# Optimization experiments

Measured on AMD Instinct MI355X. Metric: run time of the kernel, lower is better.

## Reference

```python
import jax, jax.numpy as jnp
import numpy as np

N_NODES = 40000
N_EDGES = 640000
IN_CH = 64
HID = 128
N_LAYERS = 3


def _linear_params(key, shape_in, shape_out):
    kw, kb = jax.random.split(key)
    lim = 1.0 / np.sqrt(shape_in)
    W = jax.random.uniform(kw, (shape_in, shape_out), jnp.float32, -lim, lim)
    b = jax.random.uniform(kb, (shape_out,), jnp.float32, -lim, lim)
    return W, b


def setup_inputs() -> dict:
    key = jax.random.key(0)
    ks = jax.random.split(key, 32)
    edge_index = jax.random.randint(ks[0], (2, N_EDGES), 0, N_NODES, dtype=jnp.int64 if jax.config.jax_enable_x64 else jnp.int32)
    x = jax.random.normal(ks[1], (N_NODES, IN_CH), jnp.float32)
    pos = jax.random.normal(ks[2], (N_NODES, 3), jnp.float32)
    emb_W, emb_b = _linear_params(ks[3], IN_CH, HID)

    def stack(fn):
        outs = [fn(l) for l in range(N_LAYERS)]
        Ws = jnp.stack([o[0] for o in outs])
        bs = jnp.stack([o[1] for o in outs])
        return Ws, bs

    # edge MLP: Linear(2H+1, H), SiLU, Linear(H, H), SiLU
    edge_W1, edge_b1 = stack(lambda l: _linear_params(ks[4 + l], 2 * HID + 1, HID))
    edge_W2, edge_b2 = stack(lambda l: _linear_params(ks[8 + l], HID, HID))
    # node MLP: Linear(2H, H), SiLU, Linear(H, H)
    node_W1, node_b1 = stack(lambda l: _linear_params(ks[12 + l], 2 * HID, HID))
    node_W2, node_b2 = stack(lambda l: _linear_params(ks[16 + l], HID, HID))
    # pos MLP: Linear(H, H), SiLU, Linear(H, 1)
    pos_W1, pos_b1 = stack(lambda l: _linear_params(ks[20 + l], HID, HID))
    pos_W2, pos_b2 = stack(lambda l: _linear_params(ks[24 + l], HID, 1))
    return {
        "edge_index": edge_index, "x": x, "pos": pos,
        "emb_W": emb_W, "emb_b": emb_b,
        "edge_W1": edge_W1, "edge_b1": edge_b1, "edge_W2": edge_W2, "edge_b2": edge_b2,
        "node_W1": node_W1, "node_b1": node_b1, "node_W2": node_W2, "node_b2": node_b2,
        "pos_W1": pos_W1, "pos_b1": pos_b1, "pos_W2": pos_W2, "pos_b2": pos_b2,
    }


def reference(edge_index, x, pos, emb_W, emb_b,
              edge_W1, edge_b1, edge_W2, edge_b2,
              node_W1, node_b1, node_W2, node_b2,
              pos_W1, pos_b1, pos_W2, pos_b2):
    silu = jax.nn.silu
    N = x.shape[0]
    src, dst = edge_index[0], edge_index[1]  # messages flow src -> dst
    # node embedding
    h = x @ emb_W + emb_b  # [N, H]
    # in-degree for mean aggregation of position updates
    deg = jnp.clip(jax.ops.segment_sum(jnp.ones(src.shape[0], pos.dtype), dst, num_segments=N), 1.0)
    L = edge_W1.shape[0]
    for l in range(L):
        h_i = h[dst]            # [E, H] target features
        h_j = h[src]            # [E, H] source features
        rel = pos[dst] - pos[src]  # [E, 3]
        d2 = jnp.sum(rel * rel, axis=-1, keepdims=True)  # [E, 1] squared distance
        e_in = jnp.concatenate([h_i, h_j, d2], axis=-1)  # [E, 2H+1]
        m = silu(silu(e_in @ edge_W1[l] + edge_b1[l]) @ edge_W2[l] + edge_b2[l])  # [E, H]
        agg = jax.ops.segment_sum(m, dst, num_segments=N)  # [N, H]
        n_in = jnp.concatenate([h, agg], axis=-1)  # [N, 2H]
        h = silu(n_in @ node_W1[l] + node_b1[l]) @ node_W2[l] + node_b2[l]
        # equivariant position update: pos_i += mean_j (pos_i - pos_j) * phi_x(m_ij)
        w = silu(m @ pos_W1[l] + pos_b1[l]) @ pos_W2[l] + pos_b2[l]  # [E, 1]
        pos = pos + jax.ops.segment_sum(rel * w, dst, num_segments=N) / deg[:, None]
    return h, pos
```

## Files before the change

### kernel.cpp

```cpp
#include <hip/hip_runtime.h>
#include <hip/hip_bf16.h>

#define N_NODES 40000
#define N_EDGES 640000
#define IN_CH 64
#define HID 128
#define N_LAYERS 3

typedef unsigned short u16;
typedef unsigned int u32;

typedef __attribute__((ext_vector_type(8))) __bf16 bf16x8;
typedef __attribute__((ext_vector_type(4))) float float4v;

__device__ __forceinline__ float bf2f(u16 u) {
    union { u32 i; float f; } v; v.i = ((u32)u) << 16; return v.f;
}
__device__ __forceinline__ float bflo(u32 p) {
    union { u32 i; float f; } v; v.i = p << 16; return v.f;
}
__device__ __forceinline__ float bfhi(u32 p) {
    union { u32 i; float f; } v; v.i = p & 0xffff0000u; return v.f;
}
__device__ __forceinline__ u16 f2bf(float f) {
    union { float f; u32 i; } v; v.f = f;
    u32 i = v.i;
    u32 r = (i + 0x7fffu + ((i >> 16) & 1u)) >> 16;
    return (u16)r;
}
__device__ __forceinline__ float silu_f(float x) {
    float d = 1.0f + __expf(-x);
#if __has_builtin(__builtin_amdgcn_rcpf)
    return x * __builtin_amdgcn_rcpf(d);
#else
    return __fdividef(x, d);
#endif
}

#define W_STRIDE 72
__device__ __forceinline__ void stage_w64(const u16* __restrict__ g, u16* s, int t,
                                          int chunk, int rowstride_u32) {
    const u32* gp = (const u32*)g;
    u32* sp = (u32*)s;
#pragma unroll
    for (int it = 0; it < 4; ++it) {
        int i4 = t + it * 256;
        int n = i4 >> 3, j = i4 & 7;
        *(uint4*)(sp + n * 36 + j * 4) = *(const uint4*)(gp + n * rowstride_u32 + chunk * 32 + j * 4);
    }
}
__device__ __forceinline__ void stage_w32_256(const u16* __restrict__ g, u16* s, int t, int chunk) {
    const u32* gp = (const u32*)g;
    u32* sp = (u32*)s;
#pragma unroll
    for (int it = 0; it < 4; ++it) {
        int i4 = t + it * 256;
        int o = i4 >> 2, j = i4 & 3;
        *(uint4*)(sp + o * 20 + j * 4) = *(const uint4*)(gp + o * 64 + chunk * 16 + j * 4);
    }
}

__global__ void detect_kernel(const void* __restrict__ w_raw,
                              const void* __restrict__ eidx_raw,
                              int* __restrict__ flags) {
    __shared__ int s_big, s_hi;
    if (threadIdx.x == 0) { s_big = 0; s_hi = 0; }
    __syncthreads();
    const u16* w16 = (const u16*)w_raw;
    for (int i = threadIdx.x; i < 8192; i += blockDim.x) {
        float v = bf2f(w16[i]);
        if (!(fabsf(v) <= 1.0f)) s_big = 1;
    }
    const u32* e32 = (const u32*)eidx_raw;
    for (int i = threadIdx.x; i < 256; i += blockDim.x) {
        if (e32[2 * i + 1] != 0u) s_hi = 1;
    }
    __syncthreads();
    if (threadIdx.x == 0) {
        flags[0] = s_big ? 0 : 1;
        flags[1] = s_hi ? 0 : 1;
    }
}

__global__ void cvt_f_kernel(const void* __restrict__ in, float* __restrict__ out,
                             int n, const int* __restrict__ flags) {
    int i = blockIdx.x * blockDim.x + threadIdx.x;
    if (i >= n) return;
    out[i] = flags[0] ? bf2f(((const u16*)in)[i]) : ((const float*)in)[i];
}

__global__ void cvt_idx_kernel(const void* __restrict__ in, int* __restrict__ out,
                               int n, const int* __restrict__ flags) {
    int i = blockIdx.x * blockDim.x + threadIdx.x;
    if (i >= n) return;
    out[i] = flags[1] ? (int)(((const long long*)in)[i]) : ((const int*)in)[i];
}

__global__ void tcvt_kernel(const void* __restrict__ in, u16* __restrict__ out,
                            int count, int kshift, int inLS, int outLS,
                            const int* __restrict__ flags) {
    int l = blockIdx.y;
    int i = blockIdx.x * blockDim.x + threadIdx.x;
    if (i >= count) return;
    int n = i >> kshift, k = i & ((1 << kshift) - 1);
    int si = inLS * l + k * HID + n;
    float v = flags[0] ? bf2f(((const u16*)in)[si]) : ((const float*)in)[si];
    out[(size_t)outLS * l + i] = f2bf(v);
}

__global__ void w1ab_kernel(const void* __restrict__ in, u16* __restrict__ out,
                            const int* __restrict__ flags) {
    int l = blockIdx.y;
    int i = blockIdx.x * blockDim.x + threadIdx.x;
    int o = i >> 7, k = i & 127;
    int si = l * (257 * 128) + ((o < 128) ? (k * 128 + o) : ((128 + k) * 128 + (o - 128)));
    float v = flags[0] ? bf2f(((const u16*)in)[si]) : ((const float*)in)[si];
    out[(size_t)l * 32768 + i] = f2bf(v);
}

__global__ void w1row_kernel(const void* __restrict__ in, float* __restrict__ out,
                             const int* __restrict__ flags) {
    int i = blockIdx.x * blockDim.x + threadIdx.x;
    if (i >= 384) return;
    int l = i >> 7, n = i & 127;
    int si = l * (257 * 128) + 256 * 128 + n;
    out[i] = flags[0] ? bf2f(((const u16*)in)[si]) : ((const float*)in)[si];
}

__global__ void cnt_kernel(const int* __restrict__ dst, int* __restrict__ cnt) {
    int e = blockIdx.x * blockDim.x + threadIdx.x;
    if (e < N_EDGES) atomicAdd(&cnt[dst[e]], 1);
}

__global__ __launch_bounds__(1024) void scan_kernel(const int* __restrict__ cnt,
                                                    int* __restrict__ offs) {
    __shared__ int s_part[1024];
    const int t = threadIdx.x;
    const int base = t * 40;
    int sum = 0;
    for (int j = 0; j < 40; ++j) {
        int idx = base + j;
        sum += (idx < N_NODES) ? cnt[idx] : 0;
    }
    s_part[t] = sum;
    __syncthreads();
    for (int d = 1; d < 1024; d <<= 1) {
        int v = (t >= d) ? s_part[t - d] : 0;
        __syncthreads();
        s_part[t] += v;
        __syncthreads();
    }
    int run = (t == 0) ? 0 : s_part[t - 1];
    for (int j = 0; j < 40; ++j) {
        int idx = base + j;
        if (idx < N_NODES) { offs[idx] = run; run += cnt[idx]; }
    }
    if (t == 1023) offs[N_NODES] = run;
}

__global__ void scatter_kernel(const int* __restrict__ src, const int* __restrict__ dst,
                               const int* __restrict__ offs, int* __restrict__ cur,
                               int* __restrict__ ssrc, int* __restrict__ sdst) {
    int e = blockIdx.x * blockDim.x + threadIdx.x;
    if (e >= N_EDGES) return;
    int n = dst[e];
    int p = offs[n] + atomicAdd(&cur[n], 1);
    ssrc[p] = src[e];
    sdst[p] = n;
}

__global__ void posinit_kernel(const void* __restrict__ pos_raw, float* __restrict__ posf,
                               const int* __restrict__ flags) {
    int i = blockIdx.x * blockDim.x + threadIdx.x;
    if (i < N_NODES * 3)
        posf[i] = flags[0] ? bf2f(((const u16*)pos_raw)[i]) : ((const float*)pos_raw)[i];
}

__global__ __launch_bounds__(64) void embed_kernel(
    const void* __restrict__ x_raw, const float* __restrict__ W, const float* __restrict__ b,
    u16* __restrict__ h, const int* __restrict__ flags)
{
    __shared__ float s_x[IN_CH];
    const int n = blockIdx.x;
    const int t = threadIdx.x;
    const int isbf = flags[0];
    s_x[t] = isbf ? bf2f(((const u16*)x_raw)[n * IN_CH + t])
                  : ((const float*)x_raw)[n * IN_CH + t];
    __syncthreads();
    const int o = 2 * t;
    float a0 = b[o], a1 = b[o + 1];
#pragma unroll 8
    for (int i = 0; i < IN_CH; ++i) {
        float xi = s_x[i];
        float2 w = *(const float2*)(W + i * HID + o);
        a0 = fmaf(xi, w.x, a0);
        a1 = fmaf(xi, w.y, a1);
    }
    *(u32*)(h + (size_t)n * HID + o) = (u32)f2bf(a0) | ((u32)f2bf(a1) << 16);
}

#define ACT_STRIDE 136

__global__ __launch_bounds__(256, 4) void uv_kernel(
    const u16* __restrict__ h, const u16* __restrict__ W1abt, const float* __restrict__ b1,
    u16* __restrict__ uv)
{
    __shared__ __align__(16) u16 s_a[64 * ACT_STRIDE];
    __shared__ __align__(16) u16 s_w[256 * 40];

    const int t = threadIdx.x;
    const int n0 = blockIdx.x * 64;
    const int wv = t >> 6, lane = t & 63, quad = lane >> 4, li = lane & 15;
    const int rowA = wv * 16 + li;
    const int rowC = wv * 16 + quad * 4;

    {
        int nl = t >> 2, part = t & 3;
        const uint4* hp = (const uint4*)((const u32*)h + (size_t)(n0 + nl) * 64 + part * 16);
        uint4* ap = (uint4*)((u32*)s_a + nl * (ACT_STRIDE / 2) + part * 16);
#pragma unroll
        for (int j = 0; j < 4; ++j) ap[j] = hp[j];
    }

    float4v acc[16];
#pragma unroll
    for (int ct = 0; ct < 16; ++ct) {
        float bias = (ct < 8) ? b1[ct * 16 + li] : 0.0f;
#pragma unroll
        for (int r = 0; r < 4; ++r) acc[ct][r] = bias;
    }

#pragma unroll
    for (int c = 0; c < 4; ++c) {
        if (c) __syncthreads();
        stage_w32_256(W1abt, s_w, t, c);
        __syncthreads();
        const bf16x8 av = *(const bf16x8*)(s_a + rowA * ACT_STRIDE + c * 32 + quad * 8);
#pragma unroll
        for (int ct = 0; ct < 16; ++ct) {
            const bf16x8 bv = *(const bf16x8*)(s_w + (ct * 16 + li) * 40 + quad * 8);
            acc[ct] = __builtin_amdgcn_mfma_f32_16x16x32_bf16(av, bv, acc[ct], 0, 0, 0);
        }
    }

#pragma unroll
    for (int ct = 0; ct < 16; ++ct) {
        int col = ct * 16 + li;
#pragma unroll
        for (int r = 0; r < 4; ++r)
            uv[(size_t)(n0 + rowC + r) * 256 + col] = f2bf(acc[ct][r]);
    }
}

#define TILE_E 64

__global__ __launch_bounds__(256, 4) void edge_mfma_kernel(
    const int* __restrict__ ssrc, const int* __restrict__ sdst,
    const u16* __restrict__ uv, const float* __restrict__ posf,
    const float* __restrict__ w1c_g,
    const u16* __restrict__ W2t, const float* __restrict__ b2,
    const u16* __restrict__ pW1t, const float* __restrict__ pb1,
    const float* __restrict__ pW2, const float* __restrict__ pb2,
    float* __restrict__ agg, float* __restrict__ pd)
{
    __shared__ __align__(16) u16 s_act[TILE_E * ACT_STRIDE];
    __shared__ __align__(16) u16 s_w[128 * W_STRIDE];
    __shared__ float s_w1c[128];
    __shared__ float s_d2[TILE_E];
    __shared__ float s_rel[TILE_E * 3];
    __shared__ int s_dstn[TILE_E], s_srcn[TILE_E];

    const int t = threadIdx.x;
    const int e0 = blockIdx.x * TILE_E;
    const int wv = t >> 6, lane = t & 63, quad = lane >> 4, li = lane & 15;
    const int rowA = wv * 16 + li;
    const int rowC = wv * 16 + quad * 4;

    if (t < TILE_E) {
        int e = e0 + t;
        int sN = ssrc[e], dN = sdst[e];
        s_dstn[t] = dN; s_srcn[t] = sN;
        float r0 = posf[dN * 3 + 0] - posf[sN * 3 + 0];
        float r1 = posf[dN * 3 + 1] - posf[sN * 3 + 1];
        float r2 = posf[dN * 3 + 2] - posf[sN * 3 + 2];
        s_rel[t * 3 + 0] = r0; s_rel[t * 3 + 1] = r1; s_rel[t * 3 + 2] = r2;
        s_d2[t] = r0 * r0 + r1 * r1 + r2 * r2;
    }
    if (t < 128) s_w1c[t] = w1c_g[t];
    stage_w64(W2t, s_w, t, 0, 64);
    __syncthreads();

    {
        int el = t >> 2, part = t & 3;
        int dN = s_dstn[el], sN = s_srcn[el];
        const uint4* up = (const uint4*)((const u32*)uv + (size_t)dN * 128 + part * 16);
        const uint4* vp = (const uint4*)((const u32*)uv + (size_t)sN * 128 + 64 + part * 16);
        float d2 = s_d2[el];
        u32* outp = (u32*)s_act + el * (ACT_STRIDE / 2) + part * 16;
        const float* wc = s_w1c + part * 32;
#pragma unroll
        for (int q4 = 0; q4 < 4; ++q4) {
            uint4 uu = up[q4];
            uint4 vv = vp[q4];
            u32 res[4];
#pragma unroll
            for (int j = 0; j < 4; ++j) {
                u32 ua = ((const u32*)&uu)[j], va = ((const u32*)&vv)[j];
                int col = q4 * 8 + j * 2;
                float x0 = fmaf(d2, wc[col],     bflo(ua) + bflo(va));
                float x1 = fmaf(d2, wc[col + 1], bfhi(ua) + bfhi(va));
                res[j] = (u32)f2bf(silu_f(x0)) | ((u32)f2bf(silu_f(x1)) << 16);
            }
            *(uint4*)(outp + q4 * 4) = *(uint4*)res;
        }
    }
    __syncthreads();

    float4v acc[8];
#pragma unroll
    for (int c = 0; c < 8; ++c) {
        float bias = b2[c * 16 + li];
#pragma unroll
        for (int r = 0; r < 4; ++r) acc[c][r] = bias;
    }
#pragma unroll
    for (int p = 0; p < 2; ++p) {
        if (p) {
            __syncthreads();
            stage_w64(W2t, s_w, t, 1, 64);
            __syncthreads();
        }
#pragma unroll
        for (int kk2 = 0; kk2 < 2; ++kk2) {
            const bf16x8 av = *(const bf16x8*)(s_act + rowA * ACT_STRIDE + p * 64 + kk2 * 32 + quad * 8);
#pragma unroll
            for (int c = 0; c < 8; ++c) {
                const bf16x8 bv = *(const bf16x8*)(s_w + (c * 16 + li) * W_STRIDE + kk2 * 32 + quad * 8);
                acc[c] = __builtin_amdgcn_mfma_f32_16x16x32_bf16(av, bv, acc[c], 0, 0, 0);
            }
        }
    }
    __syncthreads();

#pragma unroll
    for (int c = 0; c < 8; ++c) {
        int col = c * 16 + li;
#pragma unroll
        for (int r = 0; r < 4; ++r)
            s_act[(rowC + r) * ACT_STRIDE + col] = f2bf(silu_f(acc[c][r]));
    }
    stage_w64(pW1t, s_w, t, 0, 64);
    __syncthreads();

    {
        int c32 = t & 63, grp = t >> 6;
        int r0 = grp * 16;
        float run0 = 0.f, run1 = 0.f;
        int cur = s_dstn[r0];
        for (int r = r0; r < r0 + 16; ++r) {
            int dn = s_dstn[r];
            if (dn != cur) {
                atomicAdd(&agg[(size_t)cur * HID + 2 * c32], run0);
                atomicAdd(&agg[(size_t)cur * HID + 2 * c32 + 1], run1);
                run0 = run1 = 0.f; cur = dn;
            }
            u32 mm = *((const u32*)s_act + r * (ACT_STRIDE / 2) + c32);
            run0 += bflo(mm);
            run1 += bfhi(mm);
        }
        atomicAdd(&agg[(size_t)cur * HID + 2 * c32], run0);
        atomicAdd(&agg[(size_t)cur * HID + 2 * c32 + 1], run1);
    }

#pragma unroll
    for (int c = 0; c < 8; ++c) {
        float bias = pb1[c * 16 + li];
#pragma unroll
        for (int r = 0; r < 4; ++r) acc[c][r] = bias;
    }
#pragma unroll
    for (int p = 0; p < 2; ++p) {
        if (p) {
            __syncthreads();
            stage_w64(pW1t, s_w, t, 1, 64);
            __syncthreads();
        }
#pragma unroll
        for (int kk2 = 0; kk2 < 2; ++kk2) {
            const bf16x8 av = *(const bf16x8*)(s_act + rowA * ACT_STRIDE + p * 64 + kk2 * 32 + quad * 8);
#pragma unroll
            for (int c = 0; c < 8; ++c) {
                const bf16x8 bv = *(const bf16x8*)(s_w + (c * 16 + li) * W_STRIDE + kk2 * 32 + quad * 8);
                acc[c] = __builtin_amdgcn_mfma_f32_16x16x32_bf16(av, bv, acc[c], 0, 0, 0);
            }
        }
    }
    float part[4] = {0.f, 0.f, 0.f, 0.f};
#pragma unroll
    for (int c = 0; c < 8; ++c) {
        float pw = pW2[c * 16 + li];
#pragma unroll
        for (int r = 0; r < 4; ++r) part[r] += silu_f(acc[c][r]) * pw;
    }
#pragma unroll
    for (int r = 0; r < 4; ++r) {
        part[r] += __shfl_xor(part[r], 1, 64);
        part[r] += __shfl_xor(part[r], 2, 64);
        part[r] += __shfl_xor(part[r], 4, 64);
        part[r] += __shfl_xor(part[r], 8, 64);
    }
    __syncthreads();
    if (li == 0) {
        float pb2v = pb2[0];
#pragma unroll
        for (int r = 0; r < 4; ++r) s_d2[rowC + r] = part[r] + pb2v;
    }
    __syncthreads();
    if (t < 12) {
        int a = t % 3, grp = t / 3;
        int r0 = grp * 16;
        float run = 0.f;
        int cur = s_dstn[r0];
        for (int r = r0; r < r0 + 16; ++r) {
            int dn = s_dstn[r];
            if (dn != cur) {
                atomicAdd(&pd[(size_t)cur * 3 + a], run);
                run = 0.f; cur = dn;
            }
            run += s_rel[r * 3 + a] * s_d2[r];
        }
        atomicAdd(&pd[(size_t)cur * 3 + a], run);
    }
}

#define A_STRIDE 264

__global__ __launch_bounds__(256, 3) void node_mfma_kernel(
    const u16* __restrict__ h_in, const float* __restrict__ agg,
    const u16* __restrict__ W1t, const float* __restrict__ b1,
    const u16* __restrict__ W2t, const float* __restrict__ b2,
    u16* __restrict__ h_out,
    float* __restrict__ posf, const float* __restrict__ pd, const int* __restrict__ cnt)
{
    __shared__ __align__(16) u16 s_a[64 * A_STRIDE];
    __shared__ __align__(16) u16 s_w[128 * W_STRIDE];

    const int t = threadIdx.x;
    const int n0 = blockIdx.x * 64;
    const int wv = t >> 6, lane = t & 63, quad = lane >> 4, li = lane & 15;
    const int rowA = wv * 16 + li;
    const int rowC = wv * 16 + quad * 4;

    {
        int nl = t >> 2, part = t & 3;
        const uint4* hp = (const uint4*)((const u32*)h_in + (size_t)(n0 + nl) * 64 + part * 16);
        u32* rowp = (u32*)s_a + nl * (A_STRIDE / 2) + part * 16;
#pragma unroll
        for (int j = 0; j < 4; ++j) *(uint4*)(rowp + j * 4) = hp[j];
        const float* ap = agg + (size_t)(n0 + nl) * HID + part * 32;
        rowp += 64;
#pragma unroll
        for (int j = 0; j < 16; ++j) {
            float2 v = *(const float2*)(ap + j * 2);
            rowp[j] = (u32)f2bf(v.x) | ((u32)f2bf(v.y) << 16);
        }
    }
    stage_w64(W1t, s_w, t, 0, 128);
    __syncthreads();

    float4v acc[8];
#pragma unroll
    for (int c = 0; c < 8; ++c) {
        float bias = b1[c * 16 + li];
#pragma unroll
        for (int r = 0; r < 4; ++r) acc[c][r] = bias;
    }
#pragma unroll
    for (int p = 0; p < 4; ++p) {
        if (p) {
            __syncthreads();
            stage_w64(W1t, s_w, t, p, 128);
            __syncthreads();
        }
#pragma unroll
        for (int kk2 = 0; kk2 < 2; ++kk2) {
            const bf16x8 av = *(const bf16x8*)(s_a + rowA * A_STRIDE + p * 64 + kk2 * 32 + quad * 8);
#pragma unroll
            for (int c = 0; c < 8; ++c) {
                const bf16x8 bv = *(const bf16x8*)(s_w + (c * 16 + li) * W_STRIDE + kk2 * 32 + quad * 8);
                acc[c] = __builtin_amdgcn_mfma_f32_16x16x32_bf16(av, bv, acc[c], 0, 0, 0);
            }
        }
    }

    __syncthreads();
    u16* s_t1 = s_a;
#pragma unroll
    for (int c = 0; c < 8; ++c) {
        int col = c * 16 + li;
#pragma unroll
        for (int r = 0; r < 4; ++r)
            s_t1[(rowC + r) * ACT_STRIDE + col] = f2bf(silu_f(acc[c][r]));
    }
    stage_w64(W2t, s_w, t, 0, 64);
    __syncthreads();

#pragma unroll
    for (int c = 0; c < 8; ++c) {
        float bias = b2[c * 16 + li];
#pragma unroll
        for (int r = 0; r < 4; ++r) acc[c][r] = bias;
    }
#pragma unroll
    for (int p = 0; p < 2; ++p) {
        if (p) {
            __syncthreads();
            stage_w64(W2t, s_w, t, 1, 64);
            __syncthreads();
        }
#pragma unroll
        for (int kk2 = 0; kk2 < 2; ++kk2) {
            const bf16x8 av = *(const bf16x8*)(s_t1 + rowA * ACT_STRIDE + p * 64 + kk2 * 32 + quad * 8);
#pragma unroll
            for (int c = 0; c < 8; ++c) {
                const bf16x8 bv = *(const bf16x8*)(s_w + (c * 16 + li) * W_STRIDE + kk2 * 32 + quad * 8);
                acc[c] = __builtin_amdgcn_mfma_f32_16x16x32_bf16(av, bv, acc[c], 0, 0, 0);
            }
        }
    }

#pragma unroll
    for (int c = 0; c < 8; ++c) {
        int col = c * 16 + li;
#pragma unroll
        for (int r = 0; r < 4; ++r)
            h_out[(size_t)(n0 + rowC + r) * HID + col] = f2bf(acc[c][r]);
    }
    if (t < 192) {
        int nl = t / 3, a = t % 3;
        int n = n0 + nl;
        float dg = (float)cnt[n];
        dg = dg < 1.0f ? 1.0f : dg;
        posf[n * 3 + a] += pd[n * 3 + a] / dg;
    }
}

__global__ void out_kernel(const u16* __restrict__ h, const float* __restrict__ posf,
                           void* __restrict__ out, const int* __restrict__ flags)
{
    int i = blockIdx.x * blockDim.x + threadIdx.x;
    const int isbf = flags[0];
    if (i < N_NODES * HID) {
        if (isbf) ((u16*)out)[i] = h[i];
        else      ((float*)out)[i] = bf2f(h[i]);
    }
    if (i < N_NODES * 3) {
        if (isbf) ((u16*)out)[N_NODES * HID + i] = f2bf(posf[i]);
        else      ((float*)out)[N_NODES * HID + i] = posf[i];
    }
}

extern "C" void kernel_launch(void* const* d_in, const int* in_sizes, int n_in,
                              void* d_out, int out_size, void* d_ws, size_t ws_size,
                              hipStream_t stream) {
    (void)in_sizes; (void)n_in; (void)out_size; (void)ws_size;

    const void* eidx_raw = d_in[0];
    const void* x_raw    = d_in[1];
    const void* pos_raw  = d_in[2];
    const void* embW_raw = d_in[3];
    const void* embB_raw = d_in[4];
    const void* eW1_raw  = d_in[5];
    const void* eB1_raw  = d_in[6];
    const void* eW2_raw  = d_in[7];
    const void* eB2_raw  = d_in[8];
    const void* nW1_raw  = d_in[9];
    const void* nB1_raw  = d_in[10];
    const void* nW2_raw  = d_in[11];
    const void* nB2_raw  = d_in[12];
    const void* pW1_raw  = d_in[13];
    const void* pB1_raw  = d_in[14];
    const void* pW2_raw  = d_in[15];
    const void* pB2_raw  = d_in[16];

    float* ws   = (float*)d_ws;
    float* posf = ws;
    float* agg  = posf + (size_t)N_NODES * 3;
    float* pd   = agg + (size_t)N_NODES * HID;
    float* embW = pd + (size_t)N_NODES * 3;
    float* embB = embW + 8192;
    float* eB1f = embB + 128;
    float* eB2f = eB1f + 384;
    float* pB1f = eB2f + 384;
    float* pB2f = pB1f + 384;
    float* pW2f = pB2f + 4;
    float* W1r  = pW2f + 384;
    float* nB1f = W1r + 384;
    float* nB2f = nB1f + 384;
    float* fend = nB2f + 384;

    u16* W1abt = (u16*)fend;
    u16* W2t   = W1abt + 3 * 256 * 128;
    u16* pW1t  = W2t + 3 * 128 * 128;
    u16* nW1t  = pW1t + 3 * 128 * 128;
    u16* nW2t  = nW1t + 3 * 128 * 256;
    u16* h0    = nW2t + 3 * 128 * 128;
    u16* h1    = h0 + (size_t)N_NODES * HID;
    u16* uvb   = h1 + (size_t)N_NODES * HID;
    int* ssrc  = (int*)(uvb + (size_t)N_NODES * 256);
    int* sdst  = ssrc + N_EDGES;
    int* cnt   = sdst + N_EDGES;
    int* cur   = cnt + N_NODES;
    int* offs  = cur + N_NODES;
    int* flags = offs + N_NODES + 3;
    int* src32 = (int*)uvb;
    int* dst32 = src32 + N_EDGES;

    detect_kernel<<<1, 256, 0, stream>>>(embW_raw, eidx_raw, flags);
    cvt_idx_kernel<<<(2 * N_EDGES + 255) / 256, 256, 0, stream>>>(eidx_raw, src32, 2 * N_EDGES, flags);

    cvt_f_kernel<<<32, 256, 0, stream>>>(embW_raw, embW, 8192, flags);
    cvt_f_kernel<<<1, 128, 0, stream>>>(embB_raw, embB, 128, flags);
    cvt_f_kernel<<<2, 256, 0, stream>>>(eB1_raw, eB1f, 3 * HID, flags);
    cvt_f_kernel<<<2, 256, 0, stream>>>(eB2_raw, eB2f, 3 * HID, flags);
    cvt_f_kernel<<<2, 256, 0, stream>>>(pB1_raw, pB1f, 3 * HID, flags);
    cvt_f_kernel<<<1, 64, 0, stream>>>(pB2_raw, pB2f, 3, flags);
    cvt_f_kernel<<<2, 256, 0, stream>>>(pW2_raw, pW2f, 3 * HID, flags);
    cvt_f_kernel<<<2, 256, 0, stream>>>(nB1_raw, nB1f, 3 * HID, flags);
    cvt_f_kernel<<<2, 256, 0, stream>>>(nB2_raw, nB2f, 3 * HID, flags);
    w1row_kernel<<<2, 256, 0, stream>>>(eW1_raw, W1r, flags);

    w1ab_kernel<<<dim3(128, 3), 256, 0, stream>>>(eW1_raw, W1abt, flags);
    tcvt_kernel<<<dim3(64, 3), 256, 0, stream>>>(eW2_raw, W2t, 128 * 128, 7, 128 * 128, 128 * 128, flags);
    tcvt_kernel<<<dim3(64, 3), 256, 0, stream>>>(pW1_raw, pW1t, 128 * 128, 7, 128 * 128, 128 * 128, flags);
    tcvt_kernel<<<dim3(128, 3), 256, 0, stream>>>(nW1_raw, nW1t, 128 * 256, 8, 2 * HID * HID, 128 * 256, flags);
    tcvt_kernel<<<dim3(64, 3), 256, 0, stream>>>(nW2_raw, nW2t, 128 * 128, 7, 128 * 128, 128 * 128, flags);

    hipMemsetAsync(cnt, 0, 2 * (size_t)N_NODES * sizeof(int), stream);
    cnt_kernel<<<(N_EDGES + 255) / 256, 256, 0, stream>>>(dst32, cnt);
    scan_kernel<<<1, 1024, 0, stream>>>(cnt, offs);
    scatter_kernel<<<(N_EDGES + 255) / 256, 256, 0, stream>>>(src32, dst32, offs, cur, ssrc, sdst);

    posinit_kernel<<<(N_NODES * 3 + 255) / 256, 256, 0, stream>>>(pos_raw, posf, flags);
    embed_kernel<<<N_NODES, 64, 0, stream>>>(x_raw, embW, embB, h0, flags);

    u16* hin = h0;
    u16* hout = h1;
    for (int l = 0; l < N_LAYERS; ++l) {
        uv_kernel<<<N_NODES / 64, 256, 0, stream>>>(hin, W1abt + (size_t)l * 32768, eB1f + l * HID, uvb);
        hipMemsetAsync(agg, 0, ((size_t)N_NODES * HID + (size_t)N_NODES * 3) * sizeof(float), stream);
        edge_mfma_kernel<<<N_EDGES / TILE_E, 256, 0, stream>>>(
            ssrc, sdst, uvb, posf,
            W1r + l * HID,
            W2t + (size_t)l * 128 * 128, eB2f + l * HID,
            pW1t + (size_t)l * 128 * 128, pB1f + l * HID,
            pW2f + l * HID, pB2f + l,
            agg, pd);
        node_mfma_kernel<<<N_NODES / 64, 256, 0, stream>>>(
            hin, agg,
            nW1t + (size_t)l * 128 * 256, nB1f + l * HID,
            nW2t + (size_t)l * 128 * 128, nB2f + l * HID,
            hout, posf, pd, cnt);
        u16* tmp = hin; hin = hout; hout = tmp;
    }

    out_kernel<<<(N_NODES * HID + 255) / 256, 256, 0, stream>>>(hin, posf, d_out, flags);
}
```

Before: 887.3 us.

## Fuse embedding, uv projection, agg zeroing and output into node kernels

```diff
diff --git a/kernel.cpp b/kernel.cpp
--- a/kernel.cpp
+++ b/kernel.cpp
@@ -28,6 +28,17 @@
     u32 r = (i + 0x7fffu + ((i >> 16) & 1u)) >> 16;
     return (u16)r;
 }
+#if __has_builtin(__builtin_amdgcn_cvt_pk_bf16_f32)
+typedef __attribute__((ext_vector_type(2))) __bf16 bf16x2_t;
+__device__ __forceinline__ u32 pk2bf(float a, float b) {
+    bf16x2_t p = __builtin_amdgcn_cvt_pk_bf16_f32(a, b);
+    union { bf16x2_t v; u32 u; } c; c.v = p; return c.u;
+}
+#else
+__device__ __forceinline__ u32 pk2bf(float a, float b) {
+    return (u32)f2bf(a) | ((u32)f2bf(b) << 16);
+}
+#endif
 __device__ __forceinline__ float silu_f(float x) {
     float d = 1.0f + __expf(-x);
 #if __has_builtin(__builtin_amdgcn_rcpf)
@@ -49,16 +60,6 @@
         *(uint4*)(sp + n * 36 + j * 4) = *(const uint4*)(gp + n * rowstride_u32 + chunk * 32 + j * 4);
     }
 }
-__device__ __forceinline__ void stage_w32_256(const u16* __restrict__ g, u16* s, int t, int chunk) {
-    const u32* gp = (const u32*)g;
-    u32* sp = (u32*)s;
-#pragma unroll
-    for (int it = 0; it < 4; ++it) {
-        int i4 = t + it * 256;
-        int o = i4 >> 2, j = i4 & 3;
-        *(uint4*)(sp + o * 20 + j * 4) = *(const uint4*)(gp + o * 64 + chunk * 16 + j * 4);
-    }
-}
 
 __global__ void detect_kernel(const void* __restrict__ w_raw,
                               const void* __restrict__ eidx_raw,
@@ -82,54 +83,77 @@
     }
 }
 
-__global__ void cvt_f_kernel(const void* __restrict__ in, float* __restrict__ out,
-                             int n, const int* __restrict__ flags) {
+__global__ void small_cvt_kernel(
+    const void* __restrict__ embB_raw, const void* __restrict__ eB1_raw,
+    const void* __restrict__ eB2_raw, const void* __restrict__ pB1_raw,
+    const void* __restrict__ pB2_raw, const void* __restrict__ pW2_raw,
+    const void* __restrict__ eW1_raw, const void* __restrict__ nB1_raw,
+    const void* __restrict__ nB2_raw,
+    float* __restrict__ dstf, const int* __restrict__ flags)
+{
     int i = blockIdx.x * blockDim.x + threadIdx.x;
-    if (i >= n) return;
-    out[i] = flags[0] ? bf2f(((const u16*)in)[i]) : ((const float*)in)[i];
-}
-
-__global__ void cvt_idx_kernel(const void* __restrict__ in, int* __restrict__ out,
-                               int n, const int* __restrict__ flags) {
+    if (i >= 2820) return;
+    const void* src; int si;
+    if (i < 128)       { src = embB_raw; si = i; }
+    else if (i < 512)  { src = eB1_raw;  si = i - 128; }
+    else if (i < 896)  { src = eB2_raw;  si = i - 512; }
+    else if (i < 1280) { src = pB1_raw;  si = i - 896; }
+    else if (i < 1284) { src = pB2_raw;  si = i - 1280; if (si >= 3) { dstf[i] = 0.f; return; } }
+    else if (i < 1668) { src = pW2_raw;  si = i - 1284; }
+    else if (i < 2052) { int j = i - 1668; src = eW1_raw; si = (j >> 7) * 32896 + 32768 + (j & 127); }
+    else if (i < 2436) { src = nB1_raw;  si = i - 2052; }
+    else               { src = nB2_raw;  si = i - 2436; }
+    dstf[i] = flags[0] ? bf2f(((const u16*)src)[si]) : ((const float*)src)[si];
+}
+
+__global__ void wcvt_kernel(
+    const void* __restrict__ eW1_raw, const void* __restrict__ eW2_raw,
+    const void* __restrict__ pW1_raw, const void* __restrict__ nW1_raw,
+    const void* __restrict__ nW2_raw, const void* __restrict__ embW_raw,
+    u16* __restrict__ W1abt, u16* __restrict__ W2t, u16* __restrict__ pW1t,
+    u16* __restrict__ nW1t, u16* __restrict__ nW2t, u16* __restrict__ embWt,
+    const int* __restrict__ flags)
+{
+    int z = blockIdx.z, l = blockIdx.y;
     int i = blockIdx.x * blockDim.x + threadIdx.x;
-    if (i >= n) return;
-    out[i] = flags[1] ? (int)(((const long long*)in)[i]) : ((const int*)in)[i];
-}
-
-__global__ void tcvt_kernel(const void* __restrict__ in, u16* __restrict__ out,
-                            int count, int kshift, int inLS, int outLS,
-                            const int* __restrict__ flags) {
-    int l = blockIdx.y;
-    int i = blockIdx.x * blockDim.x + threadIdx.x;
-    if (i >= count) return;
-    int n = i >> kshift, k = i & ((1 << kshift) - 1);
-    int si = inLS * l + k * HID + n;
-    float v = flags[0] ? bf2f(((const u16*)in)[si]) : ((const float*)in)[si];
-    out[(size_t)outLS * l + i] = f2bf(v);
-}
-
-__global__ void w1ab_kernel(const void* __restrict__ in, u16* __restrict__ out,
-                            const int* __restrict__ flags) {
-    int l = blockIdx.y;
-    int i = blockIdx.x * blockDim.x + threadIdx.x;
-    int o = i >> 7, k = i & 127;
-    int si = l * (257 * 128) + ((o < 128) ? (k * 128 + o) : ((128 + k) * 128 + (o - 128)));
-    float v = flags[0] ? bf2f(((const u16*)in)[si]) : ((const float*)in)[si];
-    out[(size_t)l * 32768 + i] = f2bf(v);
-}
-
-__global__ void w1row_kernel(const void* __restrict__ in, float* __restrict__ out,
-                             const int* __restrict__ flags) {
-    int i = blockIdx.x * blockDim.x + threadIdx.x;
-    if (i >= 384) return;
-    int l = i >> 7, n = i & 127;
-    int si = l * (257 * 128) + 256 * 128 + n;
-    out[i] = flags[0] ? bf2f(((const u16*)in)[si]) : ((const float*)in)[si];
-}
-
-__global__ void cnt_kernel(const int* __restrict__ dst, int* __restrict__ cnt) {
+    const void* src; u16* dst; int si, di;
+    if (z == 0) {
+        if (i >= 32768) return;
+        int o = i >> 7, k = i & 127;
+        si = l * 32896 + ((o < 128) ? (k * 128 + o) : ((128 + k) * 128 + (o - 128)));
+        src = eW1_raw; dst = W1abt; di = l * 32768 + i;
+    } else if (z == 1) {
+        if (i >= 16384) return;
+        int n = i >> 7, k = i & 127;
+        si = l * 16384 + k * 128 + n; src = eW2_raw; dst = W2t; di = l * 16384 + i;
+    } else if (z == 2) {
+        if (i >= 16384) return;
+        int n = i >> 7, k = i & 127;
+        si = l * 16384 + k * 128 + n; src = pW1_raw; dst = pW1t; di = l * 16384 + i;
+    } else if (z == 3) {
+        if (i >= 32768) return;
+        int n = i >> 8, k = i & 255;
+        si = l * 32768 + k * 128 + n; src = nW1_raw; dst = nW1t; di = l * 32768 + i;
+    } else if (z == 4) {
+        if (i >= 16384) return;
+        int n = i >> 7, k = i & 127;
+        si = l * 16384 + k * 128 + n; src = nW2_raw; dst = nW2t; di = l * 16384 + i;
+    } else {
+        if (l != 0 || i >= 8192) return;
+        int n = i >> 6, k = i & 63;
+        si = k * 128 + n; src = embW_raw; dst = embWt; di = i;
+    }
+    float v = flags[0] ? bf2f(((const u16*)src)[si]) : ((const float*)src)[si];
+    dst[di] = f2bf(v);
+}
+
+__global__ void cnt_kernel(const void* __restrict__ eidx, int* __restrict__ cnt,
+                           const int* __restrict__ flags) {
     int e = blockIdx.x * blockDim.x + threadIdx.x;
-    if (e < N_EDGES) atomicAdd(&cnt[dst[e]], 1);
+    if (e >= N_EDGES) return;
+    int dn = flags[1] ? (int)((const long long*)eidx)[N_EDGES + e]
+                      : ((const int*)eidx)[N_EDGES + e];
+    atomicAdd(&cnt[dn], 1);
 }
 
 __global__ __launch_bounds__(1024) void scan_kernel(const int* __restrict__ cnt,
@@ -158,15 +182,23 @@
     if (t == 1023) offs[N_NODES] = run;
 }
 
-__global__ void scatter_kernel(const int* __restrict__ src, const int* __restrict__ dst,
+__global__ void scatter_kernel(const void* __restrict__ eidx,
                                const int* __restrict__ offs, int* __restrict__ cur,
-                               int* __restrict__ ssrc, int* __restrict__ sdst) {
+                               int* __restrict__ ssrc, int* __restrict__ sdst,
+                               const int* __restrict__ flags) {
     int e = blockIdx.x * blockDim.x + threadIdx.x;
     if (e >= N_EDGES) return;
-    int n = dst[e];
-    int p = offs[n] + atomicAdd(&cur[n], 1);
-    ssrc[p] = src[e];
-    sdst[p] = n;
+    int sn, dn;
+    if (flags[1]) {
+        sn = (int)((const long long*)eidx)[e];
+        dn = (int)((const long long*)eidx)[N_EDGES + e];
+    } else {
+        sn = ((const int*)eidx)[e];
+        dn = ((const int*)eidx)[N_EDGES + e];
+    }
+    int p = offs[dn] + atomicAdd(&cur[dn], 1);
+    ssrc[p] = sn;
+    sdst[p] = dn;
 }
 
 __global__ void posinit_kernel(const void* __restrict__ pos_raw, float* __restrict__ posf,
@@ -176,37 +208,16 @@
         posf[i] = flags[0] ? bf2f(((const u16*)pos_raw)[i]) : ((const float*)pos_raw)[i];
 }
 
-__global__ __launch_bounds__(64) void embed_kernel(
-    const void* __restrict__ x_raw, const float* __restrict__ W, const float* __restrict__ b,
-    u16* __restrict__ h, const int* __restrict__ flags)
+#define ACT_STRIDE 136
+
+__global__ __launch_bounds__(256, 3) void embed_uv_kernel(
+    const void* __restrict__ x_raw, const u16* __restrict__ embWt, const float* __restrict__ embB,
+    const u16* __restrict__ W1abt, const float* __restrict__ b1,
+    u16* __restrict__ h, u16* __restrict__ uv, const int* __restrict__ flags)
 {
-    __shared__ float s_x[IN_CH];
-    const int n = blockIdx.x;
-    const int t = threadIdx.x;
-    const int isbf = flags[0];
-    s_x[t] = isbf ? bf2f(((const u16*)x_raw)[n * IN_CH + t])
-                  : ((const float*)x_raw)[n * IN_CH + t];
-    __syncthreads();
-    const int o = 2 * t;
-    float a0 = b[o], a1 = b[o + 1];
-#pragma unroll 8
-    for (int i = 0; i < IN_CH; ++i) {
-        float xi = s_x[i];
-        float2 w = *(const float2*)(W + i * HID + o);
-        a0 = fmaf(xi, w.x, a0);
-        a1 = fmaf(xi, w.y, a1);
-    }
-    *(u32*)(h + (size_t)n * HID + o) = (u32)f2bf(a0) | ((u32)f2bf(a1) << 16);
-}
-
-#define ACT_STRIDE 136
-
-__global__ __launch_bounds__(256, 4) void uv_kernel(
-    const u16* __restrict__ h, const u16* __restrict__ W1abt, const float* __restrict__ b1,
-    u16* __restrict__ uv)
-{
-    __shared__ __align__(16) u16 s_a[64 * ACT_STRIDE];
-    __shared__ __align__(16) u16 s_w[256 * 40];
+    __shared__ __align__(16) u16 s_x[64 * 72];
+    __shared__ __align__(16) u16 s_h[64 * ACT_STRIDE];
+    __shared__ __align__(16) u16 s_w[128 * W_STRIDE];
 
     const int t = threadIdx.x;
     const int n0 = blockIdx.x * 64;
@@ -215,40 +226,87 @@
     const int rowC = wv * 16 + quad * 4;
 
     {
-        int nl = t >> 2, part = t & 3;
-        const uint4* hp = (const uint4*)((const u32*)h + (size_t)(n0 + nl) * 64 + part * 16);
-        uint4* ap = (uint4*)((u32*)s_a + nl * (ACT_STRIDE / 2) + part * 16);
-#pragma unroll
-        for (int j = 0; j < 4; ++j) ap[j] = hp[j];
-    }
-
-    float4v acc[16];
+        int el = t >> 2, part = t & 3;
+        u32* op = (u32*)s_x + el * 36 + part * 8;
+        if (flags[0]) {
+            const u32* xp = (const u32*)x_raw + (size_t)(n0 + el) * 32 + part * 8;
+            *(uint4*)(op)     = *(const uint4*)(xp);
+            *(uint4*)(op + 4) = *(const uint4*)(xp + 4);
+        } else {
+            const float* xp = (const float*)x_raw + (size_t)(n0 + el) * 64 + part * 16;
+#pragma unroll
+            for (int j = 0; j < 8; ++j) op[j] = pk2bf(xp[2 * j], xp[2 * j + 1]);
+        }
+    }
+    stage_w64(embWt, s_w, t, 0, 32);
+    __syncthreads();
+
+    float4v acc[8];
+#pragma unroll
+    for (int c = 0; c < 8; ++c) {
+        float bias = embB[c * 16 + li];
+#pragma unroll
+        for (int r = 0; r < 4; ++r) acc[c][r] = bias;
+    }
+#pragma unroll
+    for (int kk2 = 0; kk2 < 2; ++kk2) {
+        const bf16x8 av = *(const bf16x8*)(s_x + rowA * 72 + kk2 * 32 + quad * 8);
+#pragma unroll
+        for (int c = 0; c < 8; ++c) {
+            const bf16x8 bv = *(const bf16x8*)(s_w + (c * 16 + li) * W_STRIDE + kk2 * 32 + quad * 8);
+            acc[c] = __builtin_amdgcn_mfma_f32_16x16x32_bf16(av, bv, acc[c], 0, 0, 0);
+        }
+    }
+#pragma unroll
+    for (int c = 0; c < 8; ++c) {
+        int col = c * 16 + li;
+#pragma unroll
+        for (int r = 0; r < 4; ++r) {
+            float v = acc[c][r];
+            float vo = __shfl_xor(v, 1, 64);
+            if (!(li & 1)) {
+                u32 pkd = pk2bf(v, vo);
+                *(u32*)(s_h + (rowC + r) * ACT_STRIDE + col) = pkd;
+                *(u32*)(h + (size_t)(n0 + rowC + r) * HID + col) = pkd;
+            }
+        }
+    }
+
+    float4v a2[16];
 #pragma unroll
     for (int ct = 0; ct < 16; ++ct) {
         float bias = (ct < 8) ? b1[ct * 16 + li] : 0.0f;
 #pragma unroll
-        for (int r = 0; r < 4; ++r) acc[ct][r] = bias;
-    }
-
-#pragma unroll
-    for (int c = 0; c < 4; ++c) {
-        if (c) __syncthreads();
-        stage_w32_256(W1abt, s_w, t, c);
-        __syncthreads();
-        const bf16x8 av = *(const bf16x8*)(s_a + rowA * ACT_STRIDE + c * 32 + quad * 8);
-#pragma unroll
-        for (int ct = 0; ct < 16; ++ct) {
-            const bf16x8 bv = *(const bf16x8*)(s_w + (ct * 16 + li) * 40 + quad * 8);
-            acc[ct] = __builtin_amdgcn_mfma_f32_16x16x32_bf16(av, bv, acc[ct], 0, 0, 0);
-        }
-    }
-
+        for (int r = 0; r < 4; ++r) a2[ct][r] = bias;
+    }
+#pragma unroll
+    for (int half = 0; half < 2; ++half) {
+#pragma unroll
+        for (int chunk = 0; chunk < 2; ++chunk) {
+            __syncthreads();
+            stage_w64(W1abt + half * 16384, s_w, t, chunk, 64);
+            __syncthreads();
+#pragma unroll
+            for (int kk2 = 0; kk2 < 2; ++kk2) {
+                const bf16x8 av = *(const bf16x8*)(s_h + rowA * ACT_STRIDE + chunk * 64 + kk2 * 32 + quad * 8);
+#pragma unroll
+                for (int c = 0; c < 8; ++c) {
+                    const bf16x8 bv = *(const bf16x8*)(s_w + (c * 16 + li) * W_STRIDE + kk2 * 32 + quad * 8);
+                    a2[half * 8 + c] = __builtin_amdgcn_mfma_f32_16x16x32_bf16(av, bv, a2[half * 8 + c], 0, 0, 0);
+                }
+            }
+        }
+    }
 #pragma unroll
     for (int ct = 0; ct < 16; ++ct) {
-        int col = ct * 16 + li;
-#pragma unroll
-        for (int r = 0; r < 4; ++r)
-            uv[(size_t)(n0 + rowC + r) * 256 + col] = f2bf(acc[ct][r]);
+        int col = (ct >> 3) * 128 + (ct & 7) * 16 + li;
+#pragma unroll
+        for (int r = 0; r < 4; ++r) {
+            float v = a2[ct][r];
+            float vo = __shfl_xor(v, 1, 64);
+            if (!(li & 1))
+                *(u32*)(uv + (size_t)(n0 + rowC + r) * 256 + col) = pk2bf(v, vo);
+        }
     }
 }
 
@@ -309,7 +367,7 @@
                 int col = q4 * 8 + j * 2;
                 float x0 = fmaf(d2, wc[col],     bflo(ua) + bflo(va));
                 float x1 = fmaf(d2, wc[col + 1], bfhi(ua) + bfhi(va));
-                res[j] = (u32)f2bf(silu_f(x0)) | ((u32)f2bf(silu_f(x1)) << 16);
+                res[j] = pk2bf(silu_f(x0), silu_f(x1));
             }
             *(uint4*)(outp + q4 * 4) = *(uint4*)res;
         }
@@ -346,8 +404,12 @@
     for (int c = 0; c < 8; ++c) {
         int col = c * 16 + li;
 #pragma unroll
-        for (int r = 0; r < 4; ++r)
-            s_act[(rowC + r) * ACT_STRIDE + col] = f2bf(silu_f(acc[c][r]));
+        for (int r = 0; r < 4; ++r) {
+            float m = silu_f(acc[c][r]);
+            float mo = __shfl_xor(m, 1, 64);
+            if (!(li & 1))
+                *(u32*)(s_act + (rowC + r) * ACT_STRIDE + col) = pk2bf(m, mo);
+        }
     }
     stage_w64(pW1t, s_w, t, 0, 64);
     __syncthreads();
@@ -435,12 +497,14 @@
 
 #define A_STRIDE 264
 
-__global__ __launch_bounds__(256, 3) void node_mfma_kernel(
-    const u16* __restrict__ h_in, const float* __restrict__ agg,
+__global__ __launch_bounds__(256, 3) void node_uv_kernel(
+    const u16* __restrict__ h_in, float* __restrict__ agg,
     const u16* __restrict__ W1t, const float* __restrict__ b1,
     const u16* __restrict__ W2t, const float* __restrict__ b2,
-    u16* __restrict__ h_out,
-    float* __restrict__ posf, const float* __restrict__ pd, const int* __restrict__ cnt)
+    const u16* __restrict__ W1abt_nx, const float* __restrict__ b1_nx,
+    u16* __restrict__ h_out, u16* __restrict__ uv,
+    float* __restrict__ posf, float* __restrict__ pd, const int* __restrict__ cnt,
+    void* __restrict__ outp, const int* __restrict__ flags, int do_out)
 {
     __shared__ __align__(16) u16 s_a[64 * A_STRIDE];
     __shared__ __align__(16) u16 s_w[128 * W_STRIDE];
@@ -457,13 +521,16 @@
         u32* rowp = (u32*)s_a + nl * (A_STRIDE / 2) + part * 16;
 #pragma unroll
         for (int j = 0; j < 4; ++j) *(uint4*)(rowp + j * 4) = hp[j];
-        const float* ap = agg + (size_t)(n0 + nl) * HID + part * 32;
+        float* ap = agg + (size_t)(n0 + nl) * HID + part * 32;
         rowp += 64;
 #pragma unroll
         for (int j = 0; j < 16; ++j) {
             float2 v = *(const float2*)(ap + j * 2);
-            rowp[j] = (u32)f2bf(v.x) | ((u32)f2bf(v.y) << 16);
-        }
+            rowp[j] = pk2bf(v.x, v.y);
+        }
+        float4 z = {0.f, 0.f, 0.f, 0.f};
+#pragma unroll
+        for (int j = 0; j < 8; ++j) *(float4*)(ap + j * 4) = z;
     }
     stage_w64(W1t, s_w, t, 0, 128);
     __syncthreads();
@@ -499,8 +566,12 @@
     for (int c = 0; c < 8; ++c) {
         int col = c * 16 + li;
 #pragma unroll
-        for (int r = 0; r < 4; ++r)
-            s_t1[(rowC + r) * ACT_STRIDE + col] = f2bf(silu_f(acc[c][r]));
+        for (int r = 0; r < 4; ++r) {
+            float v = silu_f(acc[c][r]);
+            float vo = __shfl_xor(v, 1, 64);
+            if (!(li & 1))
+                *(u32*)(s_t1 + (rowC + r) * ACT_STRIDE + col) = pk2bf(v, vo);
+        }
     }
     stage_w64(W2t, s_w, t, 0, 64);
     __syncthreads();
@@ -529,34 +600,96 @@
         }
     }
 
-#pragma unroll
-    for (int c = 0; c < 8; ++c) {
-        int col = c * 16 + li;
-#pragma unroll
-        for (int r = 0; r < 4; ++r)
-            h_out[(size_t)(n0 + rowC + r) * HID + col] = f2bf(acc[c][r]);
-    }
+    if (do_out) {
+        if (flags[0]) {
+#pragma unroll
+            for (int c = 0; c < 8; ++c) {
+                int col = c * 16 + li;
+#pragma unroll
+                for (int r = 0; r < 4; ++r) {
+                    float v = acc[c][r];
+                    float vo = __shfl_xor(v, 1, 64);
+                    if (!(li & 1))
+                        *(u32*)((u16*)outp + (size_t)(n0 + rowC + r) * HID + col) = pk2bf(v, vo);
+                }
+            }
+        } else {
+#pragma unroll
+            for (int c = 0; c < 8; ++c) {
+                int col = c * 16 + li;
+#pragma unroll
+                for (int r = 0; r < 4; ++r)
+                    ((float*)outp)[(size_t)(n0 + rowC + r) * HID + col] = acc[c][r];
+            }
+        }
+    } else {
+#pragma unroll
+        for (int c = 0; c < 8; ++c) {
+            int col = c * 16 + li;
+#pragma unroll
+            for (int r = 0; r < 4; ++r) {
+                float v = acc[c][r];
+                float vo = __shfl_xor(v, 1, 64);
+                if (!(li & 1)) {
+                    u32 pkd = pk2bf(v, vo);
+                    *(u32*)(s_t1 + (rowC + r) * ACT_STRIDE + col) = pkd;
+                    *(u32*)(h_out + (size_t)(n0 + rowC + r) * HID + col) = pkd;
+                }
+            }
+        }
+    }
+
     if (t < 192) {
         int nl = t / 3, a = t % 3;
         int n = n0 + nl;
         float dg = (float)cnt[n];
         dg = dg < 1.0f ? 1.0f : dg;
-        posf[n * 3 + a] += pd[n * 3 + a] / dg;
-    }
-}
-
-__global__ void out_kernel(const u16* __restrict__ h, const float* __restrict__ posf,
-                           void* __restrict__ out, const int* __restrict__ flags)
-{
-    int i = blockIdx.x * blockDim.x + threadIdx.x;
-    const int isbf = flags[0];
-    if (i < N_NODES * HID) {
-        if (isbf) ((u16*)out)[i] = h[i];
-        else      ((float*)out)[i] = bf2f(h[i]);
-    }
-    if (i < N_NODES * 3) {
-        if (isbf) ((u16*)out)[N_NODES * HID + i] = f2bf(posf[i]);
-        else      ((float*)out)[N_NODES * HID + i] = posf[i];
+        float np = posf[n * 3 + a] + pd[n * 3 + a] / dg;
+        posf[n * 3 + a] = np;
+        pd[n * 3 + a] = 0.f;
+        if (do_out) {
+            if (flags[0]) ((u16*)outp)[(size_t)N_NODES * HID + n * 3 + a] = f2bf(np);
+            else          ((float*)outp)[(size_t)N_NODES * HID + n * 3 + a] = np;
+        }
+    }
+
+    if (do_out) return;
+
+    float4v a2[16];
+#pragma unroll
+    for (int ct = 0; ct < 16; ++ct) {
+        float bias = (ct < 8) ? b1_nx[ct * 16 + li] : 0.0f;
+#pragma unroll
+        for (int r = 0; r < 4; ++r) a2[ct][r] = bias;
+    }
+#pragma unroll
+    for (int half = 0; half < 2; ++half) {
+#pragma unroll
+        for (int chunk = 0; chunk < 2; ++chunk) {
+            __syncthreads();
+            stage_w64(W1abt_nx + half * 16384, s_w, t, chunk, 64);
+            __syncthreads();
+#pragma unroll
+            for (int kk2 = 0; kk2 < 2; ++kk2) {
+                const bf16x8 av = *(const bf16x8*)(s_t1 + rowA * ACT_STRIDE + chunk * 64 + kk2 * 32 + quad * 8);
+#pragma unroll
+                for (int c = 0; c < 8; ++c) {
+                    const bf16x8 bv = *(const bf16x8*)(s_w + (c * 16 + li) * W_STRIDE + kk2 * 32 + quad * 8);
+                    a2[half * 8 + c] = __builtin_amdgcn_mfma_f32_16x16x32_bf16(av, bv, a2[half * 8 + c], 0, 0, 0);
+                }
+            }
+        }
+    }
+#pragma unroll
+    for (int ct = 0; ct < 16; ++ct) {
+        int col = (ct >> 3) * 128 + (ct & 7) * 16 + li;
+#pragma unroll
+        for (int r = 0; r < 4; ++r) {
+            float v = a2[ct][r];
+            float vo = __shfl_xor(v, 1, 64);
+            if (!(li & 1))
+                *(u32*)(uv + (size_t)(n0 + rowC + r) * 256 + col) = pk2bf(v, vo);
+        }
     }
 }
 
@@ -587,24 +720,24 @@
     float* posf = ws;
     float* agg  = posf + (size_t)N_NODES * 3;
     float* pd   = agg + (size_t)N_NODES * HID;
-    float* embW = pd + (size_t)N_NODES * 3;
-    float* embB = embW + 8192;
-    float* eB1f = embB + 128;
-    float* eB2f = eB1f + 384;
-    float* pB1f = eB2f + 384;
-    float* pB2f = pB1f + 384;
-    float* pW2f = pB2f + 4;
-    float* W1r  = pW2f + 384;
-    float* nB1f = W1r + 384;
-    float* nB2f = nB1f + 384;
-    float* fend = nB2f + 384;
-
-    u16* W1abt = (u16*)fend;
+    float* smallf = pd + (size_t)N_NODES * 3;
+    float* embB = smallf;
+    float* eB1f = smallf + 128;
+    float* eB2f = smallf + 512;
+    float* pB1f = smallf + 896;
+    float* pB2f = smallf + 1280;
+    float* pW2f = smallf + 1284;
+    float* W1r  = smallf + 1668;
+    float* nB1f = smallf + 2052;
+    float* nB2f = smallf + 2436;
+
+    u16* W1abt = (u16*)(smallf + 2820);
     u16* W2t   = W1abt + 3 * 256 * 128;
     u16* pW1t  = W2t + 3 * 128 * 128;
     u16* nW1t  = pW1t + 3 * 128 * 128;
     u16* nW2t  = nW1t + 3 * 128 * 256;
-    u16* h0    = nW2t + 3 * 128 * 128;
+    u16* embWt = nW2t + 3 * 128 * 128;
+    u16* h0    = embWt + 8192;
     u16* h1    = h0 + (size_t)N_NODES * HID;
     u16* uvb   = h1 + (size_t)N_NODES * HID;
     int* ssrc  = (int*)(uvb + (size_t)N_NODES * 256);
@@ -613,42 +746,28 @@
     int* cur   = cnt + N_NODES;
     int* offs  = cur + N_NODES;
     int* flags = offs + N_NODES + 3;
-    int* src32 = (int*)uvb;
-    int* dst32 = src32 + N_EDGES;
 
     detect_kernel<<<1, 256, 0, stream>>>(embW_raw, eidx_raw, flags);
-    cvt_idx_kernel<<<(2 * N_EDGES + 255) / 256, 256, 0, stream>>>(eidx_raw, src32, 2 * N_EDGES, flags);
-
-    cvt_f_kernel<<<32, 256, 0, stream>>>(embW_raw, embW, 8192, flags);
-    cvt_f_kernel<<<1, 128, 0, stream>>>(embB_raw, embB, 128, flags);
-    cvt_f_kernel<<<2, 256, 0, stream>>>(eB1_raw, eB1f, 3 * HID, flags);
-    cvt_f_kernel<<<2, 256, 0, stream>>>(eB2_raw, eB2f, 3 * HID, flags);
-    cvt_f_kernel<<<2, 256, 0, stream>>>(pB1_raw, pB1f, 3 * HID, flags);
-    cvt_f_kernel<<<1, 64, 0, stream>>>(pB2_raw, pB2f, 3, flags);
-    cvt_f_kernel<<<2, 256, 0, stream>>>(pW2_raw, pW2f, 3 * HID, flags);
-    cvt_f_kernel<<<2, 256, 0, stream>>>(nB1_raw, nB1f, 3 * HID, flags);
-    cvt_f_kernel<<<2, 256, 0, stream>>>(nB2_raw, nB2f, 3 * HID, flags);
-    w1row_kernel<<<2, 256, 0, stream>>>(eW1_raw, W1r, flags);
-
-    w1ab_kernel<<<dim3(128, 3), 256, 0, stream>>>(eW1_raw, W1abt, flags);
-    tcvt_kernel<<<dim3(64, 3), 256, 0, stream>>>(eW2_raw, W2t, 128 * 128, 7, 128 * 128, 128 * 128, flags);
-    tcvt_kernel<<<dim3(64, 3), 256, 0, stream>>>(pW1_raw, pW1t, 128 * 128, 7, 128 * 128, 128 * 128, flags);
-    tcvt_kernel<<<dim3(128, 3), 256, 0, stream>>>(nW1_raw, nW1t, 128 * 256, 8, 2 * HID * HID, 128 * 256, flags);
-    tcvt_kernel<<<dim3(64, 3), 256, 0, stream>>>(nW2_raw, nW2t, 128 * 128, 7, 128 * 128, 128 * 128, flags);
+    small_cvt_kernel<<<12, 256, 0, stream>>>(embB_raw, eB1_raw, eB2_raw, pB1_raw, pB2_raw,
+                                             pW2_raw, eW1_raw, nB1_raw, nB2_raw, smallf, flags);
+    wcvt_kernel<<<dim3(128, 3, 6), 256, 0, stream>>>(
+        eW1_raw, eW2_raw, pW1_raw, nW1_raw, nW2_raw, embW_raw,
+        W1abt, W2t, pW1t, nW1t, nW2t, embWt, flags);
 
     hipMemsetAsync(cnt, 0, 2 * (size_t)N_NODES * sizeof(int), stream);
-    cnt_kernel<<<(N_EDGES + 255) / 256, 256, 0, stream>>>(dst32, cnt);
+    cnt_kernel<<<(N_EDGES + 255) / 256, 256, 0, stream>>>(eidx_raw, cnt, flags);
     scan_kernel<<<1, 1024, 0, stream>>>(cnt, offs);
-    scatter_kernel<<<(N_EDGES + 255) / 256, 256, 0, stream>>>(src32, dst32, offs, cur, ssrc, sdst);
+    scatter_kernel<<<(N_EDGES + 255) / 256, 256, 0, stream>>>(eidx_raw, offs, cur, ssrc, sdst, flags);
 
     posinit_kernel<<<(N_NODES * 3 + 255) / 256, 256, 0, stream>>>(pos_raw, posf, flags);
-    embed_kernel<<<N_NODES, 64, 0, stream>>>(x_raw, embW, embB, h0, flags);
+    hipMemsetAsync(agg, 0, ((size_t)N_NODES * HID + (size_t)N_NODES * 3) * sizeof(float), stream);
+
+    embed_uv_kernel<<<N_NODES / 64, 256, 0, stream>>>(x_raw, embWt, embB, W1abt, eB1f, h0, uvb, flags);
 
     u16* hin = h0;
     u16* hout = h1;
     for (int l = 0; l < N_LAYERS; ++l) {
-        uv_kernel<<<N_NODES / 64, 256, 0, stream>>>(hin, W1abt + (size_t)l * 32768, eB1f + l * HID, uvb);
-        hipMemsetAsync(agg, 0, ((size_t)N_NODES * HID + (size_t)N_NODES * 3) * sizeof(float), stream);
+        int last = (l == N_LAYERS - 1);
         edge_mfma_kernel<<<N_EDGES / TILE_E, 256, 0, stream>>>(
             ssrc, sdst, uvb, posf,
             W1r + l * HID,
@@ -656,13 +775,14 @@
             pW1t + (size_t)l * 128 * 128, pB1f + l * HID,
             pW2f + l * HID, pB2f + l,
             agg, pd);
-        node_mfma_kernel<<<N_NODES / 64, 256, 0, stream>>>(
+        node_uv_kernel<<<N_NODES / 64, 256, 0, stream>>>(
             hin, agg,
             nW1t + (size_t)l * 128 * 256, nB1f + l * HID,
             nW2t + (size_t)l * 128 * 128, nB2f + l * HID,
-            hout, posf, pd, cnt);
+            W1abt + (size_t)(last ? 0 : (l + 1)) * 32768, eB1f + (last ? 0 : (l + 1)) * HID,
+            hout, uvb,
+            posf, pd, cnt,
+            d_out, flags, last ? 1 : 0);
         u16* tmp = hin; hin = hout; hout = tmp;
     }
-
-    out_kernel<<<(N_NODES * HID + 255) / 256, 256, 0, stream>>>(hin, posf, d_out, flags);
-}
+}
```

After: 832.7 us. 1.07x faster.
